# Kernel optimization log

Measured on AMD Instinct MI355X. Metric: run time of the kernel, lower is better.

The kernel has to match this reference:

```python
import jax, jax.numpy as jnp
import numpy as np

B, S, F, H = 4, 1024, 256, 8
SCALE = float(F) ** 0.5  # source MULTIPLIES logits by sqrt(f)


def setup_inputs() -> dict:
    key = jax.random.key(0)
    ks = jax.random.split(key, 5)
    # 0.02 init scale keeps sigmoid logits in a non-saturated range
    return {
        "q_input": jax.random.normal(ks[0], (B, S, F), dtype=jnp.float32),
        "Wq": jax.random.normal(ks[1], (F, F * H), dtype=jnp.float32) * 0.02,
        "Wk": jax.random.normal(ks[2], (F, F * H), dtype=jnp.float32) * 0.02,
        "Wv": jax.random.normal(ks[3], (F, F * H), dtype=jnp.float32) * 0.02,
        "Wo": jax.random.normal(ks[4], (F * H, F), dtype=jnp.float32) * 0.02,
    }


def reference(q_input, Wq, Wk, Wv, Wo):
    b, s, f = q_input.shape
    h = Wq.shape[1] // f
    # kv_input is None in source -> self-attention (kv = q_input)
    q = (q_input.reshape(b * s, f) @ Wq).reshape(b, s, f, h)
    k = (q_input.reshape(b * s, f) @ Wk).reshape(b, s, f, h)
    v = (q_input.reshape(b * s, f) @ Wv).reshape(b, s, f, h)
    qkt = jnp.einsum('bifh,bjfh->bijh', q, k)          # [b, i, j, h]
    attn = jax.nn.sigmoid(qkt * SCALE)                  # sigmoid, NOT softmax
    wv = jnp.einsum('bijh,bjfh->bifh', attn, v)         # [b, i, f, h]
    wv = wv.reshape(b * s, f * h)
    out = jax.nn.relu(wv @ Wo)                          # projection + ReLU
    return out.reshape(b, s, f)
```

## Files before the change

### kernel.cpp

```cpp
#include <hip/hip_runtime.h>
#include <math.h>

#define SQ 1024
#define FQ 256
#define FH 2048

typedef _Float16 f16;
typedef f16  f16x8 __attribute__((ext_vector_type(8)));
typedef float f32x4 __attribute__((ext_vector_type(4)));

#define GLOAD_LDS16(gp, lp) \
    __builtin_amdgcn_global_load_lds((const __attribute__((address_space(1))) void*)(gp), \
                                     (__attribute__((address_space(3))) void*)(lp), 16, 0, 0)

__global__ __launch_bounds__(256) void prep_kernel(const float* __restrict__ x,
                                                   const float* __restrict__ Wq,
                                                   const float* __restrict__ Wk,
                                                   const float* __restrict__ Wv,
                                                   const float* __restrict__ Wo,
                                                   f16* __restrict__ xh,
                                                   f16* __restrict__ wqT,
                                                   f16* __restrict__ wkT,
                                                   f16* __restrict__ wvT,
                                                   f16* __restrict__ woT) {
    const int z = blockIdx.z;
    if (z == 4) {
        int id = (int)(blockIdx.x * 8 + blockIdx.y);
        int idx = (id * 256 + (int)threadIdx.x) * 8;
        float4 a = *(const float4*)(x + idx);
        float4 b = *(const float4*)(x + idx + 4);
        f16x8 v = {(f16)a.x, (f16)a.y, (f16)a.z, (f16)a.w,
                   (f16)b.x, (f16)b.y, (f16)b.z, (f16)b.w};
        *(f16x8*)(xh + idx) = v;
        return;
    }
    __shared__ f16 T[32][33];
    const int tx = threadIdx.x & 31, ty = threadIdx.x >> 5;
    if (z < 3) {
        const float* W = z == 0 ? Wq : (z == 1 ? Wk : Wv);
        f16* WT        = z == 0 ? wqT : (z == 1 ? wkT : wvT);
        const int n0 = blockIdx.x * 32, k0 = blockIdx.y * 32;
#pragma unroll
        for (int i = 0; i < 4; ++i)
            T[ty + i * 8][tx] = (f16)W[(size_t)(k0 + ty + i * 8) * FH + n0 + tx];
        __syncthreads();
#pragma unroll
        for (int i = 0; i < 4; ++i)
            WT[(size_t)(n0 + ty + i * 8) * FQ + k0 + tx] = T[tx][ty + i * 8];
    } else {
        const int n0 = (blockIdx.x >> 3) * 32;
        const int yy = (blockIdx.x & 7) * 8 + blockIdx.y;
        const int ft = yy >> 3, h = yy & 7;
#pragma unroll
        for (int i = 0; i < 4; ++i) {
            int fl = ty + i * 8;
            T[fl][tx] = (f16)Wo[(size_t)((ft * 32 + fl) * 8 + h) * FQ + n0 + tx];
        }
        __syncthreads();
#pragma unroll
        for (int i = 0; i < 4; ++i)
            woT[(size_t)(n0 + ty + i * 8) * FH + h * 256 + ft * 32 + tx] = T[tx][ty + i * 8];
    }
}

__device__ __forceinline__ void stage_sw64(const f16* __restrict__ G, int ldg,
                                           int row0, int c0, f16* S,
                                           int nrows, int w, int lane) {
    const int rsub = lane >> 3;
    const int g    = (lane & 7) ^ (rsub & 7);
#pragma unroll
    for (int rI = w; rI < (nrows >> 3); rI += 4) {
        GLOAD_LDS16(G + (size_t)(row0 + rI * 8 + rsub) * ldg + c0 + g * 8,
                    S + rI * 512);
    }
}

__device__ __forceinline__ void gemm128_sw(const f16* __restrict__ A, int lda,
                                           const f16* __restrict__ Bt, int ldb,
                                           int kbeg, int kend, f16* As, f16* Bs,
                                           f32x4 acc[4][4], int row0, int col0) {
    const int t = threadIdx.x, lane = t & 63, w = t >> 6;
    const int wr = w >> 1, wc = w & 1;
    const int lrow = lane & 15, quad = lane >> 4;
    for (int k0 = kbeg; k0 < kend; k0 += 64) {
        __syncthreads();
        stage_sw64(A, lda, row0, k0, As, 128, w, lane);
        stage_sw64(Bt, ldb, col0, k0, Bs, 128, w, lane);
        __syncthreads();
#pragma unroll
        for (int kk = 0; kk < 2; ++kk) {
            f16x8 af[4], bf[4];
#pragma unroll
            for (int i = 0; i < 4; ++i) {
                int r = wr * 64 + i * 16 + lrow;
                af[i] = *(const f16x8*)&As[r * 64 + (((kk * 4 + quad) ^ (r & 7)) << 3)];
            }
#pragma unroll
            for (int j = 0; j < 4; ++j) {
                int r = wc * 64 + j * 16 + lrow;
                bf[j] = *(const f16x8*)&Bs[r * 64 + (((kk * 4 + quad) ^ (r & 7)) << 3)];
            }
#pragma unroll
            for (int i = 0; i < 4; ++i)
#pragma unroll
                for (int j = 0; j < 4; ++j)
                    acc[i][j] = __builtin_amdgcn_mfma_f32_16x16x32_f16(af[i], bf[j], acc[i][j], 0, 0, 0);
        }
    }
}

__global__ __launch_bounds__(256) void proj_mfma(const f16* __restrict__ xh,
                                                 const f16* __restrict__ wqT,
                                                 const f16* __restrict__ wkT,
                                                 const f16* __restrict__ wvT,
                                                 f16* __restrict__ qb,
                                                 f16* __restrict__ kb,
                                                 f16* __restrict__ vb) {
    const int z = blockIdx.z;
    const f16* WT = z == 0 ? wqT : (z == 1 ? wkT : wvT);
    f16* O        = z == 0 ? qb  : (z == 1 ? kb  : vb);
    __shared__ f16 smem[17408];
    f16* As = smem;
    f16* Bs = smem + 8192;
    f32x4 acc[4][4] = {};
    const int row0 = blockIdx.y * 128, col0 = blockIdx.x * 128;
    gemm128_sw(xh, FQ, WT, FQ, 0, FQ, As, Bs, acc, row0, col0);

    __syncthreads();
    f16* Es = smem;
    const int lane = threadIdx.x & 63, w = threadIdx.x >> 6;
    const int wr = w >> 1, wc = w & 1;
    const int lrow = lane & 15, quad = lane >> 4;
    if (z != 2) {
#pragma unroll
        for (int i = 0; i < 4; ++i)
#pragma unroll
            for (int rr = 0; rr < 4; ++rr) {
                int rl = 64 * wr + 16 * i + 4 * quad + rr;
#pragma unroll
                for (int j = 0; j < 4; ++j) {
                    int cc = 64 * wc + 16 * j + lrow;
                    Es[rl * 136 + (cc & 7) * 16 + (cc >> 3)] = (f16)acc[i][j][rr];
                }
            }
        __syncthreads();
        const int f0 = col0 >> 3;
#pragma unroll
        for (int it = 0; it < 4; ++it) {
            int c = it * 256 + threadIdx.x;
            int row = c >> 3, hh = c & 7;
            int gr = row0 + row, bbb = gr >> 10, s = gr & 1023;
            f16x8 v0 = *(const f16x8*)&Es[row * 136 + hh * 16];
            f16x8 v1 = *(const f16x8*)&Es[row * 136 + hh * 16 + 8];
            f16* dst = O + ((size_t)(bbb * 8 + hh) * SQ + s) * FQ + f0;
            *(f16x8*)dst = v0;
            *(f16x8*)(dst + 8) = v1;
        }
    } else {
#pragma unroll
        for (int i = 0; i < 4; ++i)
#pragma unroll
            for (int rr = 0; rr < 4; ++rr) {
                int rl = 64 * wr + 16 * i + 4 * quad + rr;
#pragma unroll
                for (int j = 0; j < 4; ++j) {
                    int cc = 64 * wc + 16 * j + lrow;
                    Es[cc * 136 + rl] = (f16)acc[i][j][rr];
                }
            }
        __syncthreads();
        const int bbb = row0 >> 10, s0 = row0 & 1023;
#pragma unroll
        for (int it = 0; it < 8; ++it) {
            int c = it * 256 + threadIdx.x;
            int cc = c >> 4, sc = c & 15;
            int hh = cc & 7, f = (col0 >> 3) + (cc >> 3);
            f16x8 v = *(const f16x8*)&Es[cc * 136 + sc * 8];
            *(f16x8*)(O + ((size_t)(bbb * 8 + hh) * FQ + f) * SQ + s0 + sc * 8) = v;
        }
    }
}

__global__ __launch_bounds__(256) void fused_attn(const f16* __restrict__ Qb,
                                                  const f16* __restrict__ Kb,
                                                  const f16* __restrict__ Vt,
                                                  f16* __restrict__ WV) {
    __shared__ f16 smem[26752];
    f16* KB0 = smem;
    f16* KB1 = smem + 8192;
    f16* Vb  = smem + 16384;
    f16* Ps  = smem + 24576;
    const int t = threadIdx.x, lane = t & 63, w = t >> 6;
    const int wr = w >> 1, wc = w & 1;
    const int lrow = lane & 15, quad = lane >> 4;
    const int n = blockIdx.x;
    const int xcd = n & 7, rest = n >> 3;
    const int bh = xcd * 4 + (rest & 3);
    const int strip = rest >> 2;
    const int m0 = strip * 64;
    const int bb = bh >> 3, h = bh & 7;
    const f16* Qg = Qb + (size_t)bh * SQ * FQ;
    const f16* Kg = Kb + (size_t)bh * SQ * FQ;
    const f16* Vg = Vt + (size_t)bh * FQ * SQ;

    f16x8 qf[2][8];
#pragma unroll
    for (int mi = 0; mi < 2; ++mi)
#pragma unroll
        for (int ks = 0; ks < 8; ++ks)
            qf[mi][ks] = *(const f16x8*)(Qg + (size_t)(m0 + 32 * wr + 16 * mi + lrow) * FQ
                                             + ks * 32 + quad * 8);

    const int krs = lane >> 5;
    const int kgp = lane & 31;
    const int vrs = lane >> 2;
    const int vgp = lane & 3;

#pragma unroll
    for (int i = 0; i < 4; ++i) {
        int rI = w + i * 4;
        int r = rI * 2 + krs;
        GLOAD_LDS16(Kg + (size_t)r * FQ + ((kgp ^ (r & 7)) << 3), KB0 + rI * 512);
    }

    f32x4 acc_o[2][8] = {};

    for (int jt = 0; jt < 32; ++jt) {
        const int j0 = jt * 32;
        f16* KBc = (jt & 1) ? KB1 : KB0;
        f16* KBn = (jt & 1) ? KB0 : KB1;
        __syncthreads();
#pragma unroll
        for (int i = 0; i < 4; ++i) {
            int rI = w + i * 4;
            int f = rI * 16 + vrs;
            GLOAD_LDS16(Vg + (size_t)f * SQ + j0 + ((vgp ^ (f & 3)) << 3), Vb + rI * 512);
        }
        if (jt < 31) {
#pragma unroll
            for (int i = 0; i < 4; ++i) {
                int rI = w + i * 4;
                int r = rI * 2 + krs;
                GLOAD_LDS16(Kg + (size_t)(j0 + 32 + r) * FQ + ((kgp ^ (r & 7)) << 3),
                            KBn + rI * 512);
            }
        }
        f32x4 acc_s[2] = {};
#pragma unroll
        for (int ks = 0; ks < 8; ++ks) {
            int r = 16 * wc + lrow;
            f16x8 bf = *(const f16x8*)&KBc[r * 256 + (((ks * 4 + quad) ^ (r & 7)) << 3)];
#pragma unroll
            for (int mi = 0; mi < 2; ++mi)
                acc_s[mi] = __builtin_amdgcn_mfma_f32_16x16x32_f16(qf[mi][ks], bf, acc_s[mi], 0, 0, 0);
        }
#pragma unroll
        for (int mi = 0; mi < 2; ++mi)
#pragma unroll
            for (int rr = 0; rr < 4; ++rr)
                Ps[(32 * wr + 16 * mi + 4 * quad + rr) * 34 + 16 * wc + lrow] =
                    (f16)(1.0f / (1.0f + __expf(-16.0f * acc_s[mi][rr])));
        __syncthreads();
        f16x8 ap[2];
#pragma unroll
        for (int mi = 0; mi < 2; ++mi)
            ap[mi] = *(const f16x8*)&Ps[(32 * wr + 16 * mi + lrow) * 34 + quad * 8];
#pragma unroll
        for (int nj = 0; nj < 8; ++nj) {
            int f = 128 * wc + 16 * nj + lrow;
            f16x8 bv = *(const f16x8*)&Vb[f * 32 + ((quad ^ (f & 3)) << 3)];
#pragma unroll
            for (int mi = 0; mi < 2; ++mi)
                acc_o[mi][nj] = __builtin_amdgcn_mfma_f32_16x16x32_f16(
                    ap[mi], bv, acc_o[mi][nj], 0, 0, 0);
        }
    }
    __syncthreads();
    f16* Es = smem;
#pragma unroll
    for (int mi = 0; mi < 2; ++mi)
#pragma unroll
        for (int nj = 0; nj < 8; ++nj)
#pragma unroll
            for (int rr = 0; rr < 4; ++rr)
                Es[(32 * wr + 16 * mi + 4 * quad + rr) * 264 + 128 * wc + 16 * nj + lrow] =
                    (f16)acc_o[mi][nj][rr];
    __syncthreads();
#pragma unroll
    for (int it = 0; it < 8; ++it) {
        int c = it * 256 + t;
        int r = c >> 5, ck = c & 31;
        f16x8 v = *(const f16x8*)&Es[r * 264 + ck * 8];
        *(f16x8*)(WV + (size_t)(bb * SQ + m0 + r) * FH + h * 256 + ck * 8) = v;
    }
}

__global__ __launch_bounds__(256) void out_mfma8(const f16* __restrict__ WVm,
                                                 const f16* __restrict__ WoT,
                                                 float* __restrict__ PP) {
    __shared__ f16 smem[16384];
    f16* As = smem;
    f16* Bs = smem + 8192;
    f32x4 acc[4][4] = {};
    const int row0 = blockIdx.y * 128, col0 = blockIdx.x * 128;
    const int kbeg = blockIdx.z * 256;
    gemm128_sw(WVm, FH, WoT, FH, kbeg, kbeg + 256, As, Bs, acc, row0, col0);

    float* P = PP + (size_t)blockIdx.z * SQ * 4 * FQ;
    const int lane = threadIdx.x & 63, w = threadIdx.x >> 6;
    const int wr = w >> 1, wc = w & 1;
    const int lrow = lane & 15, quad = lane >> 4;
#pragma unroll
    for (int i = 0; i < 4; ++i)
#pragma unroll
        for (int rr = 0; rr < 4; ++rr) {
            int gr = row0 + wr * 64 + i * 16 + quad * 4 + rr;
#pragma unroll
            for (int j = 0; j < 4; ++j) {
                int gc = col0 + wc * 64 + j * 16 + lrow;
                P[(size_t)gr * FQ + gc] = acc[i][j][rr];
            }
        }
}

__global__ __launch_bounds__(256) void reduce_relu8(const float* __restrict__ PP,
                                                    float* __restrict__ O) {
    int idx = (blockIdx.x * 256 + threadIdx.x) * 4;
    f32x4 s = *(const f32x4*)(PP + idx);
#pragma unroll
    for (int z = 1; z < 8; ++z)
        s += *(const f32x4*)(PP + (size_t)z * 1048576 + idx);
    f32x4 r = {fmaxf(s.x, 0.f), fmaxf(s.y, 0.f), fmaxf(s.z, 0.f), fmaxf(s.w, 0.f)};
    *(f32x4*)(O + idx) = r;
}

extern "C" void kernel_launch(void* const* d_in, const int* in_sizes, int n_in,
                              void* d_out, int out_size, void* d_ws, size_t ws_size,
                              hipStream_t stream) {
    const float* x  = (const float*)d_in[0];
    const float* Wq = (const float*)d_in[1];
    const float* Wk = (const float*)d_in[2];
    const float* Wv = (const float*)d_in[3];
    const float* Wo = (const float*)d_in[4];
    float* out = (float*)d_out;

    f16* ws = (f16*)d_ws;
    f16* xh    = ws;
    f16* wqT   = xh    + 1048576;
    f16* wkT   = wqT   + 524288;
    f16* wvT   = wkT   + 524288;
    f16* woT   = wvT   + 524288;
    f16* qbuf  = woT   + 524288;
    f16* kbuf  = qbuf  + 8388608;
    f16* vbuf  = kbuf  + 8388608;
    f16* wvbuf = vbuf  + 8388608;
    float* pp  = (float*)qbuf;

    dim3 blk(256);
    prep_kernel<<<dim3(64, 8, 5), blk, 0, stream>>>(x, Wq, Wk, Wv, Wo,
                                                    xh, wqT, wkT, wvT, woT);

    proj_mfma<<<dim3(16, 32, 3), blk, 0, stream>>>(xh, wqT, wkT, wvT, qbuf, kbuf, vbuf);

    fused_attn<<<dim3(512), blk, 0, stream>>>(qbuf, kbuf, vbuf, wvbuf);

    out_mfma8<<<dim3(2, 32, 8), blk, 0, stream>>>(wvbuf, woT, pp);
    reduce_relu8<<<dim3(1024), blk, 0, stream>>>(pp, out);
}
```

Measured before the change: 198.1 us.

## Give each wave its own query rows and double-buffer V in fused attention

The attention kernel's wave decomposition changes from a 2x2 grid (32 rows by half the columns) to each wave owning 16 full query rows. Each wave now computes its own full row of scores and keeps its sigmoid tile in a private LDS slice, which removes the second block-wide barrier per key tile. V tiles are now double-buffered and prefetched alongside K, with a modified XOR swizzle. The sigmoid uses exp2 and the hardware reciprocal. In exchange, each wave reads every K and V fragment from LDS itself, so LDS read traffic goes up, and LDS use grows.

```diff
diff --git a/kernel.cpp b/kernel.cpp
--- a/kernel.cpp
+++ b/kernel.cpp
@@ -12,6 +12,8 @@
 #define GLOAD_LDS16(gp, lp) \
     __builtin_amdgcn_global_load_lds((const __attribute__((address_space(1))) void*)(gp), \
                                      (__attribute__((address_space(3))) void*)(lp), 16, 0, 0)
+
+#define SIG16(s) __builtin_amdgcn_rcpf(1.0f + __builtin_amdgcn_exp2f(-23.083120654223414f * (s)))
 
 __global__ __launch_bounds__(256) void prep_kernel(const float* __restrict__ x,
                                                    const float* __restrict__ Wq,
@@ -185,14 +187,10 @@
                                                   const f16* __restrict__ Kb,
                                                   const f16* __restrict__ Vt,
                                                   f16* __restrict__ WV) {
-    __shared__ f16 smem[26752];
-    f16* KB0 = smem;
-    f16* KB1 = smem + 8192;
-    f16* Vb  = smem + 16384;
-    f16* Ps  = smem + 24576;
+    __shared__ f16 smem[35328];
     const int t = threadIdx.x, lane = t & 63, w = t >> 6;
-    const int wr = w >> 1, wc = w & 1;
     const int lrow = lane & 15, quad = lane >> 4;
+    f16* Pw = smem + 32768 + w * 640;
     const int n = blockIdx.x;
     const int xcd = n & 7, rest = n >> 3;
     const int bh = xcd * 4 + (rest & 3);
@@ -203,13 +201,10 @@
     const f16* Kg = Kb + (size_t)bh * SQ * FQ;
     const f16* Vg = Vt + (size_t)bh * FQ * SQ;
 
-    f16x8 qf[2][8];
-#pragma unroll
-    for (int mi = 0; mi < 2; ++mi)
-#pragma unroll
-        for (int ks = 0; ks < 8; ++ks)
-            qf[mi][ks] = *(const f16x8*)(Qg + (size_t)(m0 + 32 * wr + 16 * mi + lrow) * FQ
-                                             + ks * 32 + quad * 8);
+    f16x8 qf[8];
+#pragma unroll
+    for (int ks = 0; ks < 8; ++ks)
+        qf[ks] = *(const f16x8*)(Qg + (size_t)(m0 + 16 * w + lrow) * FQ + ks * 32 + quad * 8);
 
     const int krs = lane >> 5;
     const int kgp = lane & 31;
@@ -220,23 +215,26 @@
     for (int i = 0; i < 4; ++i) {
         int rI = w + i * 4;
         int r = rI * 2 + krs;
-        GLOAD_LDS16(Kg + (size_t)r * FQ + ((kgp ^ (r & 7)) << 3), KB0 + rI * 512);
-    }
-
-    f32x4 acc_o[2][8] = {};
+        GLOAD_LDS16(Kg + (size_t)r * FQ + ((kgp ^ (r & 7)) << 3), smem + rI * 512);
+    }
+#pragma unroll
+    for (int i = 0; i < 4; ++i) {
+        int rI = w + i * 4;
+        int f = rI * 16 + vrs;
+        GLOAD_LDS16(Vg + (size_t)f * SQ + ((vgp ^ ((f >> 1) & 3)) << 3),
+                    smem + 16384 + rI * 512);
+    }
+
+    f32x4 acc_o[16] = {};
 
     for (int jt = 0; jt < 32; ++jt) {
         const int j0 = jt * 32;
-        f16* KBc = (jt & 1) ? KB1 : KB0;
-        f16* KBn = (jt & 1) ? KB0 : KB1;
-        __syncthreads();
-#pragma unroll
-        for (int i = 0; i < 4; ++i) {
-            int rI = w + i * 4;
-            int f = rI * 16 + vrs;
-            GLOAD_LDS16(Vg + (size_t)f * SQ + j0 + ((vgp ^ (f & 3)) << 3), Vb + rI * 512);
-        }
+        f16* KBc = (jt & 1) ? smem + 8192  : smem;
+        f16* VBc = (jt & 1) ? smem + 24576 : smem + 16384;
+        __syncthreads();
         if (jt < 31) {
+            f16* KBn = (jt & 1) ? smem         : smem + 8192;
+            f16* VBn = (jt & 1) ? smem + 16384 : smem + 24576;
 #pragma unroll
             for (int i = 0; i < 4; ++i) {
                 int rI = w + i * 4;
@@ -244,47 +242,44 @@
                 GLOAD_LDS16(Kg + (size_t)(j0 + 32 + r) * FQ + ((kgp ^ (r & 7)) << 3),
                             KBn + rI * 512);
             }
+#pragma unroll
+            for (int i = 0; i < 4; ++i) {
+                int rI = w + i * 4;
+                int f = rI * 16 + vrs;
+                GLOAD_LDS16(Vg + (size_t)f * SQ + j0 + 32 + ((vgp ^ ((f >> 1) & 3)) << 3),
+                            VBn + rI * 512);
+            }
         }
         f32x4 acc_s[2] = {};
 #pragma unroll
         for (int ks = 0; ks < 8; ++ks) {
-            int r = 16 * wc + lrow;
-            f16x8 bf = *(const f16x8*)&KBc[r * 256 + (((ks * 4 + quad) ^ (r & 7)) << 3)];
-#pragma unroll
-            for (int mi = 0; mi < 2; ++mi)
-                acc_s[mi] = __builtin_amdgcn_mfma_f32_16x16x32_f16(qf[mi][ks], bf, acc_s[mi], 0, 0, 0);
-        }
-#pragma unroll
-        for (int mi = 0; mi < 2; ++mi)
+#pragma unroll
+            for (int nj = 0; nj < 2; ++nj) {
+                int rk = 16 * nj + lrow;
+                f16x8 bf = *(const f16x8*)&KBc[rk * 256 + (((ks * 4 + quad) ^ (rk & 7)) << 3)];
+                acc_s[nj] = __builtin_amdgcn_mfma_f32_16x16x32_f16(qf[ks], bf, acc_s[nj], 0, 0, 0);
+            }
+        }
+#pragma unroll
+        for (int nj = 0; nj < 2; ++nj)
 #pragma unroll
             for (int rr = 0; rr < 4; ++rr)
-                Ps[(32 * wr + 16 * mi + 4 * quad + rr) * 34 + 16 * wc + lrow] =
-                    (f16)(1.0f / (1.0f + __expf(-16.0f * acc_s[mi][rr])));
-        __syncthreads();
-        f16x8 ap[2];
-#pragma unroll
-        for (int mi = 0; mi < 2; ++mi)
-            ap[mi] = *(const f16x8*)&Ps[(32 * wr + 16 * mi + lrow) * 34 + quad * 8];
-#pragma unroll
-        for (int nj = 0; nj < 8; ++nj) {
-            int f = 128 * wc + 16 * nj + lrow;
-            f16x8 bv = *(const f16x8*)&Vb[f * 32 + ((quad ^ (f & 3)) << 3)];
-#pragma unroll
-            for (int mi = 0; mi < 2; ++mi)
-                acc_o[mi][nj] = __builtin_amdgcn_mfma_f32_16x16x32_f16(
-                    ap[mi], bv, acc_o[mi][nj], 0, 0, 0);
+                Pw[(4 * quad + rr) * 40 + 16 * nj + lrow] = (f16)SIG16(acc_s[nj][rr]);
+        f16x8 ap = *(const f16x8*)&Pw[lrow * 40 + quad * 8];
+#pragma unroll
+        for (int nj = 0; nj < 16; ++nj) {
+            int f = 16 * nj + lrow;
+            f16x8 bv = *(const f16x8*)&VBc[f * 32 + ((quad ^ ((f >> 1) & 3)) << 3)];
+            acc_o[nj] = __builtin_amdgcn_mfma_f32_16x16x32_f16(ap, bv, acc_o[nj], 0, 0, 0);
         }
     }
     __syncthreads();
     f16* Es = smem;
 #pragma unroll
-    for (int mi = 0; mi < 2; ++mi)
-#pragma unroll
-        for (int nj = 0; nj < 8; ++nj)
-#pragma unroll
-            for (int rr = 0; rr < 4; ++rr)
-                Es[(32 * wr + 16 * mi + 4 * quad + rr) * 264 + 128 * wc + 16 * nj + lrow] =
-                    (f16)acc_o[mi][nj][rr];
+    for (int nj = 0; nj < 16; ++nj)
+#pragma unroll
+        for (int rr = 0; rr < 4; ++rr)
+            Es[(16 * w + 4 * quad + rr) * 264 + 16 * nj + lrow] = (f16)acc_o[nj][rr];
     __syncthreads();
 #pragma unroll
     for (int it = 0; it < 8; ++it) {
```

After: 184.4 us. -6.9%, faster.
